# Kernel tuning notes

Hardware: AMD Instinct MI355X
Metric: run time of the kernel (lower is better)

The kernel has to match this reference:

```python
import jax, jax.numpy as jnp
import numpy as np

D, H, W = 160, 192, 160


def _grid_sample_3d(vol, grid):
    """torch F.grid_sample (3D, bilinear/trilinear, padding='zeros', align_corners=False).
    vol: [B,C,D,H,W]; grid: [B,Do,Ho,Wo,3], last dim ordered (x,y,z) in [-1,1]."""
    B, C, Dv, Hv, Wv = vol.shape
    x, y, z = grid[..., 0], grid[..., 1], grid[..., 2]
    # align_corners=False unnormalization
    ix = ((x + 1.0) * Wv - 1.0) * 0.5
    iy = ((y + 1.0) * Hv - 1.0) * 0.5
    iz = ((z + 1.0) * Dv - 1.0) * 0.5
    fx, fy, fz = jnp.floor(ix), jnp.floor(iy), jnp.floor(iz)
    wx, wy, wz = ix - fx, iy - fy, iz - fz
    ix0, iy0, iz0 = fx.astype(jnp.int32), fy.astype(jnp.int32), fz.astype(jnp.int32)
    vol_flat = vol.reshape(B, C, Dv * Hv * Wv)
    out_sp = x.shape[1:]  # (Do, Ho, Wo)

    def gather(zi, yi, xi):
        inb = ((zi >= 0) & (zi < Dv) & (yi >= 0) & (yi < Hv) & (xi >= 0) & (xi < Wv))
        lin = ((jnp.clip(zi, 0, Dv - 1) * Hv + jnp.clip(yi, 0, Hv - 1)) * Wv
               + jnp.clip(xi, 0, Wv - 1)).reshape(B, -1)
        vals = jax.vmap(lambda v, i: v[:, i])(vol_flat, lin)  # [B,C,N]
        return vals.reshape((B, C) + out_sp) * inb[:, None].astype(vol.dtype)

    out = jnp.zeros((B, C) + tuple(out_sp), vol.dtype)
    # fixed 8-corner trilinear accumulation
    for dz, wz_ in ((0, 1.0 - wz), (1, wz)):
        for dy, wy_ in ((0, 1.0 - wy), (1, wy)):
            for dx, wx_ in ((0, 1.0 - wx), (1, wx)):
                w = (wz_ * wy_ * wx_)[:, None]  # [B,1,Do,Ho,Wo]
                out = out + w * gather(iz0 + dz, iy0 + dy, ix0 + dx)
    return out


def _voxel_grid():
    gd, gh, gw = jnp.meshgrid(jnp.arange(D, dtype=jnp.float32),
                              jnp.arange(H, dtype=jnp.float32),
                              jnp.arange(W, dtype=jnp.float32), indexing='ij')
    return jnp.stack([gd, gh, gw])[None]  # [1,3,D,H,W], channels (d,h,w)


def _to_xyz(t):
    # [B,3,D,H,W] channels (d,h,w) -> [B,D,H,W,3] channels (x,y,z)
    return jnp.moveaxis(t, 1, -1)[..., ::-1]


def setup_inputs() -> dict:
    key = jax.random.key(0)
    k1, k2, k3 = jax.random.split(key, 3)
    src = jax.random.normal(k1, (1, 1, D, H, W), dtype=jnp.float32)
    flow1 = jax.random.normal(k2, (1, 3, D, H, W), dtype=jnp.float32)
    flow2 = jax.random.normal(k3, (1, 3, D, H, W), dtype=jnp.float32)
    range_flow = jnp.float32(0.4)
    return {"src": src, "flow1": flow1, "flow2": flow2, "range_flow": range_flow}


def reference(src, flow1, flow2, range_flow):
    grid = _voxel_grid()  # voxel-coordinate identity grid
    # NOTE: grid2 is intentionally NOT normalized to [-1,1] (faithful to source quirk)
    grid2 = _to_xyz(grid + flow2 * range_flow)
    flow1_warped = _grid_sample_3d(flow1, grid2)
    out_flow = flow1_warped + flow2
    denom = jnp.array([D - 1, H - 1, W - 1], jnp.float32).reshape(1, 3, 1, 1, 1)
    new_locs_total = 2.0 * ((grid + out_flow * range_flow) / denom - 0.5)
    deform_2_img = _grid_sample_3d(src, _to_xyz(new_locs_total))
    return deform_2_img, out_flow
```

## Files before the change

### kernel.cpp

```cpp
#include <hip/hip_runtime.h>

constexpr int Dv = 160, Hv = 192, Wv = 160;
constexpr int NN = Dv * Hv * Wv;

constexpr int TW = 32, TH = 8, TD = 8;
constexpr int SX = 40, SY = 13, SZ = 13;
constexpr int SLEN = SX * SY * SZ;
constexpr int SVEC = SLEN / 4;
constexpr int SITER = (SVEC + 255) / 256;
constexpr int SPAD = SITER * 256 * 4;

__device__ __forceinline__ void tri3_rare(const float* __restrict__ v,
                                          float gx, float gy, float gz,
                                          float& o0, float& o1, float& o2) {
  o0 = 0.0f; o1 = 0.0f; o2 = 0.0f;
  float ix = ((gx + 1.0f) * (float)Wv - 1.0f) * 0.5f;
  float iy = ((gy + 1.0f) * (float)Hv - 1.0f) * 0.5f;
  float iz = ((gz + 1.0f) * (float)Dv - 1.0f) * 0.5f;
  float fx = floorf(ix), fy = floorf(iy), fz = floorf(iz);
  int x0 = (int)fx, y0 = (int)fy, z0 = (int)fz;
  if (x0 < -1 || x0 >= Wv || y0 < -1 || y0 >= Hv || z0 < -1 || z0 >= Dv)
    return;
  float wx = ix - fx, wy = iy - fy, wz = iz - fz;
#pragma unroll
  for (int c = 0; c < 8; ++c) {
    const int dz = (c >> 2) & 1, dy = (c >> 1) & 1, dx = c & 1;
    int zi = z0 + dz, yi = y0 + dy, xi = x0 + dx;
    if ((unsigned)zi < (unsigned)Dv && (unsigned)yi < (unsigned)Hv &&
        (unsigned)xi < (unsigned)Wv) {
      float wgt = (dz ? wz : 1.0f - wz) * (dy ? wy : 1.0f - wy) *
                  (dx ? wx : 1.0f - wx);
      int lin = (zi * Hv + yi) * Wv + xi;
      o0 += wgt * v[lin];
      o1 += wgt * v[NN + lin];
      o2 += wgt * v[2 * NN + lin];
    }
  }
}

__global__ __launch_bounds__(256)
void st_tiled_kernel(const float* __restrict__ src,
                     const float* __restrict__ flow1,
                     const float* __restrict__ flow2,
                     const float* __restrict__ rfp,
                     float* __restrict__ out) {
  __shared__ float tile[SPAD];

  const int tid = threadIdx.x;
  const int bx0 = blockIdx.x * TW;
  const int by0 = blockIdx.y * TH;
  const int bz0 = blockIdx.z * TD;
  const float rf = rfp[0];

  const int lw = tid & (TW - 1);
  const int lh = tid >> 5;
  const int w = bx0 + lw;
  const int h = by0 + lh;

  float f2d[TD], f2h[TD], f2w[TD];
#pragma unroll
  for (int ld = 0; ld < TD; ++ld) {
    int idx = ((bz0 + ld) * Hv + h) * Wv + w;
    f2d[ld] = flow2[idx];
    f2h[ld] = flow2[NN + idx];
    f2w[ld] = flow2[2 * NN + idx];
  }

  const int bxo = bx0 - 4, byo = by0 - 2, bzo = bz0 - 2;
#pragma unroll
  for (int i = 0; i < SITER; ++i) {
    int t = tid + i * 256;
    int tt = (i == SITER - 1) ? min(t, SVEC - 1) : t;
    int e = tt * 4;
    int tz = e / (SY * SX);
    int r = e - tz * (SY * SX);
    int ty = r / SX;
    int tx = r - ty * SX;
    int gx = min(max(bxo + tx, 0), Wv - 4);
    int gy = min(max(byo + ty, 0), Hv - 1);
    int gz = min(max(bzo + tz, 0), Dv - 1);
    int g = (gz * Hv + gy) * Wv + gx;
    __builtin_amdgcn_global_load_lds(
        (const __attribute__((address_space(1))) void*)(src + g),
        (__attribute__((address_space(3))) void*)(tile + e), 16, 0, 0);
  }
  __syncthreads();

  const float wf = (float)w, hf = (float)h;
  constexpr float KX = (float)Wv / (float)(Wv - 1);
  constexpr float KY = (float)Hv / (float)(Hv - 1);
  constexpr float KZ = (float)Dv / (float)(Dv - 1);

#pragma unroll
  for (int ld = 0; ld < TD; ++ld) {
    const int d = bz0 + ld;
    const float df = (float)d;
    const int idx = (d * Hv + h) * Wv + w;

    float a0, a1, a2;
    tri3_rare(flow1, wf + rf * f2w[ld], hf + rf * f2h[ld], df + rf * f2d[ld],
              a0, a1, a2);

    float of_d = a0 + f2d[ld];
    float of_h = a1 + f2h[ld];
    float of_w = a2 + f2w[ld];

    out[NN + idx] = of_d;
    out[2 * NN + idx] = of_h;
    out[3 * NN + idx] = of_w;

    float ix = (wf + rf * of_w) * KX - 0.5f;
    float iy = (hf + rf * of_h) * KY - 0.5f;
    float iz = (df + rf * of_d) * KZ - 0.5f;

    float fx = floorf(ix), fy = floorf(iy), fz = floorf(iz);
    float wx = ix - fx, wy = iy - fy, wz = iz - fz;
    int x0 = (int)fx, y0 = (int)fy, z0 = (int)fz;

    float wx0 = ((unsigned)x0 < (unsigned)Wv) ? (1.0f - wx) : 0.0f;
    float wx1 = ((unsigned)(x0 + 1) < (unsigned)Wv) ? wx : 0.0f;
    float wy0 = ((unsigned)y0 < (unsigned)Hv) ? (1.0f - wy) : 0.0f;
    float wy1 = ((unsigned)(y0 + 1) < (unsigned)Hv) ? wy : 0.0f;
    float wz0 = ((unsigned)z0 < (unsigned)Dv) ? (1.0f - wz) : 0.0f;
    float wz1 = ((unsigned)(z0 + 1) < (unsigned)Dv) ? wz : 0.0f;

    int xa0 = min(max(x0, 0), Wv - 1), xa1 = min(max(x0 + 1, 0), Wv - 1);
    int ya0 = min(max(y0, 0), Hv - 1), ya1 = min(max(y0 + 1, 0), Hv - 1);

    int za1 = min(max(z0 + 1, 0), Dv - 1);
    int r10 = (za1 * Hv + ya0) * Wv;
    int r11 = (za1 * Hv + ya1) * Wv;
    float v100 = src[r10 + xa0], v101 = src[r10 + xa1];
    float v110 = src[r11 + xa0], v111 = src[r11 + xa1];

    int txi = x0 - bxo, tyi = y0 - byo, tzi = z0 - bzo;
    bool fast = ((unsigned)txi <= (unsigned)(SX - 2)) &
                ((unsigned)tyi <= (unsigned)(SY - 2)) &
                ((unsigned)tzi <= (unsigned)(SZ - 1));

    float v000, v001, v010, v011;
    if (fast) {
      int base = (tzi * SY + tyi) * SX + txi;
      v000 = tile[base];
      v001 = tile[base + 1];
      v010 = tile[base + SX];
      v011 = tile[base + SX + 1];
    } else {
      int za0 = min(max(z0, 0), Dv - 1);
      int r00 = (za0 * Hv + ya0) * Wv;
      int r01 = (za0 * Hv + ya1) * Wv;
      v000 = src[r00 + xa0]; v001 = src[r00 + xa1];
      v010 = src[r01 + xa0]; v011 = src[r01 + xa1];
    }

    float c00 = v000 * wx0 + v001 * wx1;
    float c01 = v010 * wx0 + v011 * wx1;
    float c10 = v100 * wx0 + v101 * wx1;
    float c11 = v110 * wx0 + v111 * wx1;
    float c0 = c00 * wy0 + c01 * wy1;
    float c1 = c10 * wy0 + c11 * wy1;
    out[idx] = c0 * wz0 + c1 * wz1;
  }
}

extern "C" void kernel_launch(void* const* d_in, const int* in_sizes, int n_in,
                              void* d_out, int out_size, void* d_ws, size_t ws_size,
                              hipStream_t stream) {
  const float* src   = (const float*)d_in[0];
  const float* flow1 = (const float*)d_in[1];
  const float* flow2 = (const float*)d_in[2];
  const float* rfp   = (const float*)d_in[3];
  float* out = (float*)d_out;

  dim3 grid(Wv / TW, Hv / TH, Dv / TD);
  hipLaunchKernelGGL(st_tiled_kernel, grid, dim3(256), 0, stream,
                     src, flow1, flow2, rfp, out);
}
```

Measured before the change: 187.0 us.

## Vectorize flow loads and output stores as float4, read all corners from LDS

Threads now each handle four consecutive x voxels in two depth slices, instead of one x voxel across eight slices. This allows float4 loads of flow2 and float4 stores of all four outputs. The fast path now reads all eight trilinear corners from the LDS tile (z bound tightened to SZ-2) rather than fetching the upper z-plane corners from global memory. It trades fewer, wider memory transactions and less global traffic for more per-thread register state and a different LDS access pattern that may raise bank conflicts.

```diff
diff --git a/kernel.cpp b/kernel.cpp
--- a/kernel.cpp
+++ b/kernel.cpp
@@ -52,18 +52,20 @@
   const int bz0 = blockIdx.z * TD;
   const float rf = rfp[0];
 
-  const int lw = tid & (TW - 1);
-  const int lh = tid >> 5;
-  const int w = bx0 + lw;
-  const int h = by0 + lh;
+  const int lx = tid & 7;
+  const int ly = (tid >> 3) & 7;
+  const int lz = tid >> 6;
+  const int w0 = bx0 + lx * 4;
+  const int h = by0 + ly;
 
-  float f2d[TD], f2h[TD], f2w[TD];
+  float4 f2d4[2], f2h4[2], f2w4[2];
 #pragma unroll
-  for (int ld = 0; ld < TD; ++ld) {
-    int idx = ((bz0 + ld) * Hv + h) * Wv + w;
-    f2d[ld] = flow2[idx];
-    f2h[ld] = flow2[NN + idx];
-    f2w[ld] = flow2[2 * NN + idx];
+  for (int s = 0; s < 2; ++s) {
+    int d = bz0 + 2 * lz + s;
+    int idx = (d * Hv + h) * Wv + w0;
+    f2d4[s] = *(const float4*)(flow2 + idx);
+    f2h4[s] = *(const float4*)(flow2 + NN + idx);
+    f2w4[s] = *(const float4*)(flow2 + 2 * NN + idx);
   }
 
   const int bxo = bx0 - 4, byo = by0 - 2, bzo = bz0 - 2;
@@ -86,80 +88,94 @@
   }
   __syncthreads();
 
-  const float wf = (float)w, hf = (float)h;
+  const float hf = (float)h;
   constexpr float KX = (float)Wv / (float)(Wv - 1);
   constexpr float KY = (float)Hv / (float)(Hv - 1);
   constexpr float KZ = (float)Dv / (float)(Dv - 1);
 
 #pragma unroll
-  for (int ld = 0; ld < TD; ++ld) {
-    const int d = bz0 + ld;
+  for (int s = 0; s < 2; ++s) {
+    const int d = bz0 + 2 * lz + s;
     const float df = (float)d;
-    const int idx = (d * Hv + h) * Wv + w;
+    const int idx = (d * Hv + h) * Wv + w0;
 
-    float a0, a1, a2;
-    tri3_rare(flow1, wf + rf * f2w[ld], hf + rf * f2h[ld], df + rf * f2d[ld],
-              a0, a1, a2);
+    float4 def, ofd4, ofh4, ofw4;
+#pragma unroll
+    for (int j = 0; j < 4; ++j) {
+      const float wf = (float)(w0 + j);
+      const float f2dv = (&f2d4[s].x)[j];
+      const float f2hv = (&f2h4[s].x)[j];
+      const float f2wv = (&f2w4[s].x)[j];
 
-    float of_d = a0 + f2d[ld];
-    float of_h = a1 + f2h[ld];
-    float of_w = a2 + f2w[ld];
+      float a0, a1, a2;
+      tri3_rare(flow1, wf + rf * f2wv, hf + rf * f2hv, df + rf * f2dv,
+                a0, a1, a2);
 
-    out[NN + idx] = of_d;
-    out[2 * NN + idx] = of_h;
-    out[3 * NN + idx] = of_w;
+      float of_d = a0 + f2dv;
+      float of_h = a1 + f2hv;
+      float of_w = a2 + f2wv;
+      (&ofd4.x)[j] = of_d;
+      (&ofh4.x)[j] = of_h;
+      (&ofw4.x)[j] = of_w;
 
-    float ix = (wf + rf * of_w) * KX - 0.5f;
-    float iy = (hf + rf * of_h) * KY - 0.5f;
-    float iz = (df + rf * of_d) * KZ - 0.5f;
+      float ix = (wf + rf * of_w) * KX - 0.5f;
+      float iy = (hf + rf * of_h) * KY - 0.5f;
+      float iz = (df + rf * of_d) * KZ - 0.5f;
 
-    float fx = floorf(ix), fy = floorf(iy), fz = floorf(iz);
-    float wx = ix - fx, wy = iy - fy, wz = iz - fz;
-    int x0 = (int)fx, y0 = (int)fy, z0 = (int)fz;
+      float fx = floorf(ix), fy = floorf(iy), fz = floorf(iz);
+      float wx = ix - fx, wy = iy - fy, wz = iz - fz;
+      int x0 = (int)fx, y0 = (int)fy, z0 = (int)fz;
 
-    float wx0 = ((unsigned)x0 < (unsigned)Wv) ? (1.0f - wx) : 0.0f;
-    float wx1 = ((unsigned)(x0 + 1) < (unsigned)Wv) ? wx : 0.0f;
-    float wy0 = ((unsigned)y0 < (unsigned)Hv) ? (1.0f - wy) : 0.0f;
-    float wy1 = ((unsigned)(y0 + 1) < (unsigned)Hv) ? wy : 0.0f;
-    float wz0 = ((unsigned)z0 < (unsigned)Dv) ? (1.0f - wz) : 0.0f;
-    float wz1 = ((unsigned)(z0 + 1) < (unsigned)Dv) ? wz : 0.0f;
+      float wx0 = ((unsigned)x0 < (unsigned)Wv) ? (1.0f - wx) : 0.0f;
+      float wx1 = ((unsigned)(x0 + 1) < (unsigned)Wv) ? wx : 0.0f;
+      float wy0 = ((unsigned)y0 < (unsigned)Hv) ? (1.0f - wy) : 0.0f;
+      float wy1 = ((unsigned)(y0 + 1) < (unsigned)Hv) ? wy : 0.0f;
+      float wz0 = ((unsigned)z0 < (unsigned)Dv) ? (1.0f - wz) : 0.0f;
+      float wz1 = ((unsigned)(z0 + 1) < (unsigned)Dv) ? wz : 0.0f;
 
-    int xa0 = min(max(x0, 0), Wv - 1), xa1 = min(max(x0 + 1, 0), Wv - 1);
-    int ya0 = min(max(y0, 0), Hv - 1), ya1 = min(max(y0 + 1, 0), Hv - 1);
+      int txi = x0 - bxo, tyi = y0 - byo, tzi = z0 - bzo;
+      bool fast = ((unsigned)txi <= (unsigned)(SX - 2)) &
+                  ((unsigned)tyi <= (unsigned)(SY - 2)) &
+                  ((unsigned)tzi <= (unsigned)(SZ - 2));
 
-    int za1 = min(max(z0 + 1, 0), Dv - 1);
-    int r10 = (za1 * Hv + ya0) * Wv;
-    int r11 = (za1 * Hv + ya1) * Wv;
-    float v100 = src[r10 + xa0], v101 = src[r10 + xa1];
-    float v110 = src[r11 + xa0], v111 = src[r11 + xa1];
+      float v000, v001, v010, v011, v100, v101, v110, v111;
+      if (fast) {
+        int base = (tzi * SY + tyi) * SX + txi;
+        v000 = tile[base];
+        v001 = tile[base + 1];
+        v010 = tile[base + SX];
+        v011 = tile[base + SX + 1];
+        v100 = tile[base + SY * SX];
+        v101 = tile[base + SY * SX + 1];
+        v110 = tile[base + SY * SX + SX];
+        v111 = tile[base + SY * SX + SX + 1];
+      } else {
+        int xa0 = min(max(x0, 0), Wv - 1), xa1 = min(max(x0 + 1, 0), Wv - 1);
+        int ya0 = min(max(y0, 0), Hv - 1), ya1 = min(max(y0 + 1, 0), Hv - 1);
+        int za0 = min(max(z0, 0), Dv - 1), za1 = min(max(z0 + 1, 0), Dv - 1);
+        int r00 = (za0 * Hv + ya0) * Wv;
+        int r01 = (za0 * Hv + ya1) * Wv;
+        int r10 = (za1 * Hv + ya0) * Wv;
+        int r11 = (za1 * Hv + ya1) * Wv;
+        v000 = src[r00 + xa0]; v001 = src[r00 + xa1];
+        v010 = src[r01 + xa0]; v011 = src[r01 + xa1];
+        v100 = src[r10 + xa0]; v101 = src[r10 + xa1];
+        v110 = src[r11 + xa0]; v111 = src[r11 + xa1];
+      }
 
-    int txi = x0 - bxo, tyi = y0 - byo, tzi = z0 - bzo;
-    bool fast = ((unsigned)txi <= (unsigned)(SX - 2)) &
-                ((unsigned)tyi <= (unsigned)(SY - 2)) &
-                ((unsigned)tzi <= (unsigned)(SZ - 1));
-
-    float v000, v001, v010, v011;
-    if (fast) {
-      int base = (tzi * SY + tyi) * SX + txi;
-      v000 = tile[base];
-      v001 = tile[base + 1];
-      v010 = tile[base + SX];
-      v011 = tile[base + SX + 1];
-    } else {
-      int za0 = min(max(z0, 0), Dv - 1);
-      int r00 = (za0 * Hv + ya0) * Wv;
-      int r01 = (za0 * Hv + ya1) * Wv;
-      v000 = src[r00 + xa0]; v001 = src[r00 + xa1];
-      v010 = src[r01 + xa0]; v011 = src[r01 + xa1];
+      float c00 = v000 * wx0 + v001 * wx1;
+      float c01 = v010 * wx0 + v011 * wx1;
+      float c10 = v100 * wx0 + v101 * wx1;
+      float c11 = v110 * wx0 + v111 * wx1;
+      float c0 = c00 * wy0 + c01 * wy1;
+      float c1 = c10 * wy0 + c11 * wy1;
+      (&def.x)[j] = c0 * wz0 + c1 * wz1;
     }
 
-    float c00 = v000 * wx0 + v001 * wx1;
-    float c01 = v010 * wx0 + v011 * wx1;
-    float c10 = v100 * wx0 + v101 * wx1;
-    float c11 = v110 * wx0 + v111 * wx1;
-    float c0 = c00 * wy0 + c01 * wy1;
-    float c1 = c10 * wy0 + c11 * wy1;
-    out[idx] = c0 * wz0 + c1 * wz1;
+    *(float4*)(out + idx) = def;
+    *(float4*)(out + NN + idx) = ofd4;
+    *(float4*)(out + 2 * NN + idx) = ofh4;
+    *(float4*)(out + 3 * NN + idx) = ofw4;
   }
 }
 
```

New measurement: 179.4 us. -4.1%, faster.
